# Performance work log

Measured on AMD Instinct MI355X. Metric: run time of the kernel, lower is better.

Reference implementation:

```python
import jax, jax.numpy as jnp
import numpy as np

P = 16          # patch size
GH = GW = 29    # grid (464/16)
N = GH * GW     # 841 tokens
E = 384         # embed dim
NH = 6          # heads
HD = E // NH    # 64
DEPTH = 8
EPS = 1e-5


def _dist_bias():
    g = jnp.linspace(0.0, 1.0, GH)
    gy, gx = jnp.meshgrid(g, g, indexing='ij')
    coords = jnp.stack([gy.ravel(), gx.ravel()], axis=-1)        # [N,2]
    d2 = ((coords[None, :, :] - coords[:, None, :]) ** 2).sum(-1)  # [N,N]
    return -d2 / d2.max()                                        # in [-1,0]


def _ln(x, g, b):
    m = x.mean(-1, keepdims=True)
    v = ((x - m) ** 2).mean(-1, keepdims=True)
    return (x - m) * jax.lax.rsqrt(v + EPS) * g + b


def _shift(x, dy, dx):
    # zero-pad shift, matching F.pad default 'constant' mode in the source
    B, C, H, W = x.shape
    if dy > 0:
        x = jnp.pad(x, ((0, 0), (0, 0), (dy, 0), (0, 0)))[:, :, :H, :]
    elif dy < 0:
        x = jnp.pad(x, ((0, 0), (0, 0), (0, -dy), (0, 0)))[:, :, -H:, :]
    if dx > 0:
        x = jnp.pad(x, ((0, 0), (0, 0), (0, 0), (dx, 0)))[:, :, :, :W]
    elif dx < 0:
        x = jnp.pad(x, ((0, 0), (0, 0), (0, 0), (0, -dx)))[:, :, :, -W:]
    return x


def _patchify(x):
    B, C, H, W = x.shape
    gh, gw = H // P, W // P
    x = x.reshape(B, C, gh, P, gw, P)
    x = x.transpose(0, 2, 4, 1, 3, 5)         # [B,gh,gw,C,p,p]
    return x.reshape(B, gh * gw, C * P * P)


def setup_inputs() -> dict:
    key = jax.random.key(0)
    ks = jax.random.split(key, 8)
    D = DEPTH
    s = 0.02
    inp = {
        'x': jax.random.normal(ks[0], (16, 3, 464, 464), jnp.float32),
        'tok_ng': jnp.ones((3840,), jnp.float32),
        'tok_nb': jnp.zeros((3840,), jnp.float32),
        'tok_w1': jax.random.normal(ks[1], (3840, 768), jnp.float32) * s,
        'tok_b1': jnp.zeros((768,), jnp.float32),
        'tok_w2': jax.random.normal(ks[2], (768, 384), jnp.float32) * s,
        'tok_b2': jnp.zeros((384,), jnp.float32),
        'ln1_g': jnp.ones((D, E), jnp.float32),
        'ln1_b': jnp.zeros((D, E), jnp.float32),
        'w_qkv': jax.random.normal(ks[3], (D, E, 3 * E), jnp.float32) * s,
        'temp': jnp.full((D, NH), np.log(HD ** -0.5), jnp.float32),
        'loc_w': jnp.full((D, NH), 0.1, jnp.float32),
        'w_proj': jax.random.normal(ks[4], (D, E, E), jnp.float32) * s,
        'b_proj': jnp.zeros((D, E), jnp.float32),
        'ls1': jnp.full((D, E), 1e-4, jnp.float32),
        'ln2_g': jnp.ones((D, E), jnp.float32),
        'ln2_b': jnp.zeros((D, E), jnp.float32),
        'ff_w1': jax.random.normal(ks[5], (D, E, 4 * E), jnp.float32) * s,
        'ff_b1': jnp.zeros((D, 4 * E), jnp.float32),
        'ff_w2': jax.random.normal(ks[6], (D, 4 * E, E), jnp.float32) * s,
        'ff_b2': jnp.zeros((D, E), jnp.float32),
        'ls2': jnp.full((D, E), 1e-4, jnp.float32),
    }
    return inp


def _forward(x, tok_ng, tok_nb, tok_w1, tok_b1, tok_w2, tok_b2,
             ln1_g, ln1_b, w_qkv, temp, loc_w, w_proj, b_proj, ls1,
             ln2_g, ln2_b, ff_w1, ff_b1, ff_w2, ff_b2, ls2):
    p2 = P // 2
    shifts = [x, _shift(x, p2, 0), _shift(x, -p2, 0), _shift(x, 0, p2), _shift(x, 0, -p2)]
    patches = jnp.concatenate([_patchify(s) for s in shifts], axis=-1)  # [B,N,3840]
    h = _ln(patches, tok_ng, tok_nb)
    h = jax.nn.gelu(h @ tok_w1 + tok_b1, approximate=False)
    h = h @ tok_w2 + tok_b2                                             # [B,N,E]

    loc = _dist_bias()                                                  # [N,N]

    def block(h, p):
        (g1, b1, wqkv, tp, lw, wp, bp, l1, g2, b2, fw1, fb1, fw2, fb2, l2) = p
        y = _ln(h, g1, b1)
        qkv = (y @ wqkv).reshape(h.shape[0], N, 3, NH, HD)
        qkv = qkv.transpose(2, 0, 3, 1, 4)                              # [3,B,H,N,hd]
        q, k, v = qkv[0], qkv[1], qkv[2]
        scale = jnp.exp(tp)[:, None, None]                              # per-head temperature
        logits = jnp.einsum('bhnd,bhmd->bhnm', q, k) * scale
        logits = logits + lw[:, None, None] * loc                       # per-head locality bias
        a = jax.nn.softmax(logits, axis=-1)
        o = jnp.einsum('bhnm,bhmd->bhnd', a, v)
        o = o.transpose(0, 2, 1, 3).reshape(h.shape[0], N, E)
        h = h + l1 * (o @ wp + bp)
        y2 = _ln(h, g2, b2)
        f = jax.nn.gelu(y2 @ fw1 + fb1, approximate=False) @ fw2 + fb2
        h = h + l2 * f
        return h, None

    params = (ln1_g, ln1_b, w_qkv, temp, loc_w, w_proj, b_proj, ls1,
              ln2_g, ln2_b, ff_w1, ff_b1, ff_w2, ff_b2, ls2)
    h, _ = jax.lax.scan(block, h, params)
    return h


def reference(x, tok_ng, tok_nb, tok_w1, tok_b1, tok_w2, tok_b2,
              ln1_g, ln1_b, w_qkv, temp, loc_w, w_proj, b_proj, ls1,
              ln2_g, ln2_b, ff_w1, ff_b1, ff_w2, ff_b2, ls2):
    return _forward(x, tok_ng, tok_nb, tok_w1, tok_b1, tok_w2, tok_b2,
                    ln1_g, ln1_b, w_qkv, temp, loc_w, w_proj, b_proj, ls1,
                    ln2_g, ln2_b, ff_w1, ff_b1, ff_w2, ff_b2, ls2)
```

## Files before the change

### kernel.cpp

```cpp
#include <hip/hip_runtime.h>
#include <math.h>

typedef __attribute__((ext_vector_type(8))) short short8;
typedef __attribute__((ext_vector_type(4))) float f32x4;
typedef unsigned short u16;

#define NTOK 841
#define GRID_H 29
#define E_ 384
#define NH_ 6
#define MROWS 13456
#define MP 13568
#define MQ 14336
#define CM 5120

__device__ __forceinline__ u16 f2bf(float f) {
  union { float f; unsigned int u; } c; c.f = f;
  unsigned int u = c.u;
  return (u16)((u + 0x7fffu + ((u >> 16) & 1u)) >> 16);
}

__device__ __forceinline__ float bf2f(u16 b) {
  union { unsigned int u; float f; } c; c.u = ((unsigned int)b) << 16; return c.f;
}

__device__ __forceinline__ float gelu_exact(float v) {
  return 0.5f * v * (1.f + erff(v * 0.70710678118654752440f));
}

__device__ __forceinline__ float fexp2(float x) {
  float r; asm("v_exp_f32 %0, %1" : "=v"(r) : "v"(x)); return r;
}

__device__ __forceinline__ int swz64(int row, int col) {
  return row * 128 + ((((col >> 3) ^ (row & 7)) << 4) | ((col & 7) << 1));
}

__global__ __launch_bounds__(256) void transpose_conv(const float* __restrict__ in,
    u16* __restrict__ out, int K, int N) {
  __shared__ float tile[32][33];
  size_t zo = (size_t)blockIdx.z * K * N;
  const float* inp = in + zo;
  u16* outp = out + zo;
  int n0 = blockIdx.x * 32, k0 = blockIdx.y * 32;
  int tx = threadIdx.x & 31, ty = threadIdx.x >> 5;
  #pragma unroll
  for (int r = ty; r < 32; r += 8) tile[r][tx] = inp[(size_t)(k0 + r) * N + n0 + tx];
  __syncthreads();
  #pragma unroll
  for (int r = ty; r < 32; r += 8) outp[(size_t)(n0 + r) * K + k0 + tx] = f2bf(tile[tx][r]);
}

__global__ __launch_bounds__(256) void patch_ln(const float* __restrict__ x,
    const float* __restrict__ g, const float* __restrict__ bsh, u16* __restrict__ out,
    int t0) {
  int t = t0 + blockIdx.x;
  int tid = threadIdx.x;
  u16* orow = out + (size_t)blockIdx.x * 3840;
  if (t >= MROWS) {
    #pragma unroll
    for (int j = 0; j < 15; ++j) orow[tid + j * 256] = 0;
    return;
  }
  int bimg = t / NTOK, n = t % NTOK;
  int gy = n / GRID_H, gx = n % GRID_H;
  float vals[15];
  float s1 = 0.f, s2 = 0.f;
  #pragma unroll
  for (int j = 0; j < 15; ++j) {
    int cout = tid + j * 256;
    int s = cout / 768, rem = cout % 768;
    int c = rem / 256, rem2 = rem % 256;
    int py = rem2 / 16, px = rem2 % 16;
    int dy = (s == 1 ? 8 : 0) - (s == 2 ? 8 : 0);
    int dx = (s == 3 ? 8 : 0) - (s == 4 ? 8 : 0);
    int Y = gy * 16 + py - dy;
    int X = gx * 16 + px - dx;
    float v = 0.f;
    if (Y >= 0 && Y < 464 && X >= 0 && X < 464)
      v = x[(((size_t)bimg * 3 + c) * 464 + Y) * 464 + X];
    vals[j] = v;
    s1 += v; s2 += v * v;
  }
  #pragma unroll
  for (int m = 1; m < 64; m <<= 1) { s1 += __shfl_xor(s1, m); s2 += __shfl_xor(s2, m); }
  __shared__ float ws1[4], ws2[4];
  int wid = tid >> 6;
  if ((tid & 63) == 0) { ws1[wid] = s1; ws2[wid] = s2; }
  __syncthreads();
  s1 = ws1[0] + ws1[1] + ws1[2] + ws1[3];
  s2 = ws2[0] + ws2[1] + ws2[2] + ws2[3];
  float mean = s1 * (1.f / 3840.f);
  float var = s2 * (1.f / 3840.f) - mean * mean;
  float rs = rsqrtf(var + 1e-5f);
  #pragma unroll
  for (int j = 0; j < 15; ++j) {
    int cout = tid + j * 256;
    orow[cout] = f2bf((vals[j] - mean) * rs * g[cout] + bsh[cout]);
  }
}

__global__ __launch_bounds__(256) void ln384(const float* __restrict__ h,
    const float* __restrict__ g, const float* __restrict__ bsh, u16* __restrict__ y) {
  int row = blockIdx.x * 4 + (threadIdx.x >> 6);
  int lane = threadIdx.x & 63;
  const float* hr = h + (size_t)row * E_;
  float v[6];
  float s1 = 0.f;
  #pragma unroll
  for (int j = 0; j < 6; ++j) { v[j] = hr[lane + j * 64]; s1 += v[j]; }
  #pragma unroll
  for (int m = 1; m < 64; m <<= 1) s1 += __shfl_xor(s1, m);
  float mean = s1 * (1.f / 384.f);
  float s2 = 0.f;
  #pragma unroll
  for (int j = 0; j < 6; ++j) { float d = v[j] - mean; s2 += d * d; }
  #pragma unroll
  for (int m = 1; m < 64; m <<= 1) s2 += __shfl_xor(s2, m);
  float rs = rsqrtf(s2 * (1.f / 384.f) + 1e-5f);
  u16* yr = y + (size_t)row * E_;
  #pragma unroll
  for (int j = 0; j < 6; ++j) {
    int c = lane + j * 64;
    yr[c] = f2bf((v[j] - mean) * rs * g[c] + bsh[c]);
  }
}

__global__ __launch_bounds__(256) void ln384p(const float* __restrict__ h,
    const float* __restrict__ g, const float* __restrict__ bsh, u16* __restrict__ yp) {
  int rowp = blockIdx.x * 4 + (threadIdx.x >> 6);
  int lane = threadIdx.x & 63;
  int bg = rowp / 896, tk = rowp - bg * 896;
  u16* yr = yp + (size_t)rowp * E_;
  if (tk >= NTOK) {
    #pragma unroll
    for (int j = 0; j < 6; ++j) yr[lane + j * 64] = 0;
    return;
  }
  const float* hr = h + (size_t)(bg * NTOK + tk) * E_;
  float v[6];
  float s1 = 0.f;
  #pragma unroll
  for (int j = 0; j < 6; ++j) { v[j] = hr[lane + j * 64]; s1 += v[j]; }
  #pragma unroll
  for (int m = 1; m < 64; m <<= 1) s1 += __shfl_xor(s1, m);
  float mean = s1 * (1.f / 384.f);
  float s2 = 0.f;
  #pragma unroll
  for (int j = 0; j < 6; ++j) { float d = v[j] - mean; s2 += d * d; }
  #pragma unroll
  for (int m = 1; m < 64; m <<= 1) s2 += __shfl_xor(s2, m);
  float rs = rsqrtf(s2 * (1.f / 384.f) + 1e-5f);
  #pragma unroll
  for (int j = 0; j < 6; ++j) {
    int c = lane + j * 64;
    yr[c] = f2bf((v[j] - mean) * rs * g[c] + bsh[c]);
  }
}

template<int EPI, int TM>
__global__ __launch_bounds__(256) void gemm_bt(
    const u16* __restrict__ A, const u16* __restrict__ BT,
    int N, int K,
    const float* __restrict__ bias, const float* __restrict__ lscale,
    float* __restrict__ resid, u16* __restrict__ outb, float* __restrict__ outf) {
  constexpr int MI = TM / 32;
  constexpr int BUF = (TM + 128) * 64;
  __shared__ alignas(16) char smem[2 * BUF * 2];
  short* As = (short*)smem;
  const int gx = gridDim.x;
  const int nwg = gx * gridDim.y;
  int L = blockIdx.x + blockIdx.y * gx;
  int q8 = nwg >> 3, r8 = nwg & 7, xcd = L & 7, pos = L >> 3;
  int L2 = (xcd < r8 ? xcd * (q8 + 1) : r8 * (q8 + 1) + (xcd - r8) * q8) + pos;
  const int m0 = (L2 / gx) * TM, n0 = (L2 % gx) * 128;
  const int tid = threadIdx.x;
  const int lane = tid & 63, wid = tid >> 6;
  const int wm = wid >> 1, wn = wid & 1;
  const int rowl = lane >> 3;
  const int colc = (((lane & 7) ^ (rowl & 7)) << 3);
  f32x4 acc[MI][4] = {};
  const int nkt = K >> 6;

  auto stage = [&](int b, int kt) {
    short* Ab = As + b * BUF;
    short* Bb = Ab + TM * 64;
    const int k0 = kt * 64;
    #pragma unroll
    for (int i = 0; i < TM / 32; ++i) {
      int chunk = i * 4 + wid;
      const u16* ga = A + (size_t)(m0 + chunk * 8 + rowl) * K + k0 + colc;
      __builtin_amdgcn_global_load_lds((const __attribute__((address_space(1))) void*)ga,
          (__attribute__((address_space(3))) void*)(Ab + (chunk << 9)), 16, 0, 0);
    }
    #pragma unroll
    for (int i = 0; i < 4; ++i) {
      int chunk = i * 4 + wid;
      const u16* gb = BT + (size_t)(n0 + chunk * 8 + rowl) * K + k0 + colc;
      __builtin_amdgcn_global_load_lds((const __attribute__((address_space(1))) void*)gb,
          (__attribute__((address_space(3))) void*)(Bb + (chunk << 9)), 16, 0, 0);
    }
  };

  stage(0, 0);
  for (int kt = 0; kt < nkt; ++kt) {
    const int cur = kt & 1;
    if (kt + 1 < nkt) {
      stage(cur ^ 1, kt + 1);
      if (TM == 128) asm volatile("s_waitcnt vmcnt(8)" ::: "memory");
      else           asm volatile("s_waitcnt vmcnt(6)" ::: "memory");
    } else {
      asm volatile("s_waitcnt vmcnt(0)" ::: "memory");
    }
    __builtin_amdgcn_s_barrier();
    __builtin_amdgcn_sched_barrier(0);
    short* Ab = As + cur * BUF;
    short* Bb = Ab + TM * 64;
    #pragma unroll
    for (int kk = 0; kk < 2; ++kk) {
      short8 a[MI], bfr[4];
      #pragma unroll
      for (int mi = 0; mi < MI; ++mi) {
        int ra = wm * (TM / 2) + mi * 16 + (lane & 15);
        a[mi] = *(const short8*)(Ab + ra * 64 + ((((kk << 2) | (lane >> 4)) ^ (ra & 7)) << 3));
      }
      #pragma unroll
      for (int nj = 0; nj < 4; ++nj) {
        int rb = wn * 64 + nj * 16 + (lane & 15);
        bfr[nj] = *(const short8*)(Bb + rb * 64 + ((((kk << 2) | (lane >> 4)) ^ (rb & 7)) << 3));
      }
      #pragma unroll
      for (int mi = 0; mi < MI; ++mi)
        #pragma unroll
        for (int nj = 0; nj < 4; ++nj)
          acc[mi][nj] = __builtin_amdgcn_mfma_f32_16x16x32_bf16(a[mi], bfr[nj], acc[mi][nj], 0, 0, 0);
    }
    __builtin_amdgcn_s_barrier();
  }
  const int rrow = (lane >> 4) << 2;
  const int ccol = lane & 15;
  if (EPI == 1) {
    u16* Cs = (u16*)smem;
    __syncthreads();
    #pragma unroll
    for (int mi = 0; mi < MI; ++mi)
      #pragma unroll
      for (int nj = 0; nj < 4; ++nj) {
        int cc = wn * 64 + nj * 16 + ccol;
        float bi = bias[n0 + cc];
        #pragma unroll
        for (int r = 0; r < 4; ++r) {
          int cr = wm * (TM / 2) + mi * 16 + rrow + r;
          Cs[cr * 136 + cc] = f2bf(gelu_exact(acc[mi][nj][r] + bi));
        }
      }
    __syncthreads();
    #pragma unroll
    for (int it = 0; it < TM / 16; ++it) {
      int idx = it * 256 + tid;
      int orow = idx >> 4, c = idx & 15;
      short8 v = *(const short8*)(Cs + orow * 136 + c * 8);
      *(short8*)(outb + (size_t)(m0 + orow) * N + n0 + c * 8) = v;
    }
    return;
  }
  #pragma unroll
  for (int mi = 0; mi < MI; ++mi)
    #pragma unroll
    for (int nj = 0; nj < 4; ++nj) {
      int gn = n0 + wn * 64 + nj * 16 + ccol;
      #pragma unroll
      for (int r = 0; r < 4; ++r) {
        int gm = m0 + wm * (TM / 2) + mi * 16 + rrow + r;
        float v = acc[mi][nj][r];
        if (EPI == 2) {
          outf[(size_t)gm * N + gn] = v + bias[gn];
        } else {
          float* p = resid + (size_t)gm * N + gn;
          *p = *p + lscale[gn] * (v + bias[gn]);
        }
      }
    }
}

__global__ __launch_bounds__(256) void gemm_qkv(
    const u16* __restrict__ A, const u16* __restrict__ BT,
    u16* __restrict__ Qp, u16* __restrict__ Kp, u16* __restrict__ Vp) {
  const int K = 384;
  constexpr int BUF = 256 * 64;
  __shared__ alignas(16) char smem[2 * BUF * 2];
  short* As = (short*)smem;
  int L = blockIdx.x + blockIdx.y * 9;
  int L2 = (L & 7) * 126 + (L >> 3);
  const int m0 = (L2 / 9) * 128, n0 = (L2 % 9) * 128;
  const int tid = threadIdx.x;
  const int lane = tid & 63, wid = tid >> 6;
  const int wm = wid >> 1, wn = wid & 1;
  const int rowl = lane >> 3;
  const int colc = (((lane & 7) ^ (rowl & 7)) << 3);
  f32x4 acc[4][4] = {};

  auto stage = [&](int b, int kt) {
    short* Ab = As + b * BUF;
    short* Bb = Ab + 128 * 64;
    const int k0 = kt * 64;
    #pragma unroll
    for (int i = 0; i < 4; ++i) {
      int chunk = i * 4 + wid;
      const u16* ga = A + (size_t)(m0 + chunk * 8 + rowl) * K + k0 + colc;
      __builtin_amdgcn_global_load_lds((const __attribute__((address_space(1))) void*)ga,
          (__attribute__((address_space(3))) void*)(Ab + (chunk << 9)), 16, 0, 0);
      const u16* gb = BT + (size_t)(n0 + chunk * 8 + rowl) * K + k0 + colc;
      __builtin_amdgcn_global_load_lds((const __attribute__((address_space(1))) void*)gb,
          (__attribute__((address_space(3))) void*)(Bb + (chunk << 9)), 16, 0, 0);
    }
  };

  stage(0, 0);
  for (int kt = 0; kt < 6; ++kt) {
    const int cur = kt & 1;
    if (kt + 1 < 6) {
      stage(cur ^ 1, kt + 1);
      asm volatile("s_waitcnt vmcnt(8)" ::: "memory");
    } else {
      asm volatile("s_waitcnt vmcnt(0)" ::: "memory");
    }
    __builtin_amdgcn_s_barrier();
    __builtin_amdgcn_sched_barrier(0);
    short* Ab = As + cur * BUF;
    short* Bb = Ab + 128 * 64;
    #pragma unroll
    for (int kk = 0; kk < 2; ++kk) {
      short8 a[4], bfr[4];
      #pragma unroll
      for (int mi = 0; mi < 4; ++mi) {
        int ra = wm * 64 + mi * 16 + (lane & 15);
        a[mi] = *(const short8*)(Ab + ra * 64 + ((((kk << 2) | (lane >> 4)) ^ (ra & 7)) << 3));
      }
      #pragma unroll
      for (int nj = 0; nj < 4; ++nj) {
        int rb = wn * 64 + nj * 16 + (lane & 15);
        bfr[nj] = *(const short8*)(Bb + rb * 64 + ((((kk << 2) | (lane >> 4)) ^ (rb & 7)) << 3));
      }
      #pragma unroll
      for (int mi = 0; mi < 4; ++mi)
        #pragma unroll
        for (int nj = 0; nj < 4; ++nj)
          acc[mi][nj] = __builtin_amdgcn_mfma_f32_16x16x32_bf16(a[mi], bfr[nj], acc[mi][nj], 0, 0, 0);
    }
    __builtin_amdgcn_s_barrier();
  }
  const int seg = n0 / 384;
  const int h0 = (n0 - seg * 384) >> 6;
  const int bg = m0 / 896;
  const int tk0 = m0 - bg * 896;
  const int rrow = (lane >> 4) << 2;
  const int ccol = lane & 15;
  u16* Cs = (u16*)smem;
  __syncthreads();
  #pragma unroll
  for (int mi = 0; mi < 4; ++mi)
    #pragma unroll
    for (int nj = 0; nj < 4; ++nj) {
      int cc = wn * 64 + nj * 16 + ccol;
      #pragma unroll
      for (int r = 0; r < 4; ++r) {
        int cr = wm * 64 + mi * 16 + rrow + r;
        u16 bv = f2bf(acc[mi][nj][r]);
        if (seg == 2) Cs[cc * 136 + cr] = bv;
        else          Cs[cr * 136 + cc] = bv;
      }
    }
  __syncthreads();
  #pragma unroll
  for (int i = 0; i < 8; ++i) {
    int idx = i * 256 + tid;
    int c = idx & 7;
    int orow = idx >> 3;
    int hs = orow >> 7;
    int rl = orow & 127;
    size_t bh = (size_t)(bg * 6 + h0 + hs);
    if (seg == 2) {
      int tile_l = rl >> 6, hd = rl & 63;
      short8 v = *(const short8*)(Cs + (hs * 64 + hd) * 136 + tile_l * 64 + c * 8);
      int tile = (tk0 >> 6) + tile_l;
      *(short8*)(Vp + bh * 57344 + tile * 4096 + hd * 64 + ((c ^ (hd & 7)) << 3)) = v;
    } else {
      short8 v = *(const short8*)(Cs + rl * 136 + hs * 64 + c * 8);
      if (seg == 0) {
        *(short8*)(Qp + (bh * 896 + tk0 + rl) * 64 + c * 8) = v;
      } else {
        int tok = tk0 + rl;
        *(short8*)(Kp + bh * 57344 + (tok >> 6) * 4096 + (tok & 63) * 64 + ((c ^ (tok & 7)) << 3)) = v;
      }
    }
  }
}

__global__ __launch_bounds__(256) void attn_sk(const u16* __restrict__ Qp,
    const u16* __restrict__ Kp, const u16* __restrict__ Vp,
    const float* __restrict__ temp_d, const float* __restrict__ locw_d,
    u16* __restrict__ op, float* __restrict__ ml) {
  int Lw = blockIdx.x;
  int L2 = (Lw & 7) * 336 + (Lw >> 3);
  const int bh = L2 / 28;
  const int rem = L2 % 28;
  const int ks = rem / 14, qt = rem % 14;
  const int hh = bh % NH_;
  const int tid = threadIdx.x, lane = tid & 63, w = tid >> 6;
  const int lg = lane >> 4, lc = lane & 15;
  const float LOG2E = 1.44269504088896f;
  const float scale = __expf(temp_d[hh]) * LOG2E;
  const float lwh = locw_d[hh] * LOG2E * -0.5f;
  const int kb0 = ks * 448;

  __shared__ alignas(16) char ktl[2][8192];
  __shared__ alignas(16) char vtl[2][8192];
  __shared__ alignas(16) char pl[4][2048];
  __shared__ float yx2[896 * 2];

  for (int j = tid; j < 896; j += 256) {
    unsigned jc = j < NTOK ? (unsigned)j : (NTOK - 1);
    yx2[j * 2]     = (float)(jc / 29u) * (1.f / 28.f);
    yx2[j * 2 + 1] = (float)(jc % 29u) * (1.f / 28.f);
  }

  const char* qb = (const char*)(Qp + ((size_t)bh * 896 + qt * 64) * 64);
  short8 qf0 = *(const short8*)(qb + (w * 16 + lc) * 128 + lg * 16);
  short8 qf1 = *(const short8*)(qb + (w * 16 + lc) * 128 + 64 + lg * 16);

  const char* kbase = (const char*)Kp + ((size_t)bh * 14 + ks * 7) * 8192;
  const char* vbase = (const char*)Vp + ((size_t)bh * 14 + ks * 7) * 8192;

  auto stage = [&](int b, int kt) {
    #pragma unroll
    for (int i = 0; i < 2; ++i) {
      int off = (i * 4 + w) * 1024;
      __builtin_amdgcn_global_load_lds(
          (const __attribute__((address_space(1))) void*)(kbase + kt * 8192 + off + lane * 16),
          (__attribute__((address_space(3))) void*)(ktl[b] + off), 16, 0, 0);
      __builtin_amdgcn_global_load_lds(
          (const __attribute__((address_space(1))) void*)(vbase + kt * 8192 + off + lane * 16),
          (__attribute__((address_space(3))) void*)(vtl[b] + off), 16, 0, 0);
    }
  };

  f32x4 of[4] = {};
  float mrow[4], psum[4];
  #pragma unroll
  for (int r = 0; r < 4; ++r) { mrow[r] = -3e38f; psum[r] = 0.f; }

  stage(0, 0);
  asm volatile("s_waitcnt vmcnt(0)" ::: "memory");
  __syncthreads();

  float qy[4], qx[4];
  #pragma unroll
  for (int r = 0; r < 4; ++r) {
    int iq = qt * 64 + w * 16 + (lg << 2) + r;
    qy[r] = yx2[iq * 2];
    qx[r] = yx2[iq * 2 + 1];
  }

  for (int kt = 0; kt < 7; ++kt) {
    const int b = kt & 1;
    if (kt < 6) stage(b ^ 1, kt + 1);

    const char* kb = ktl[b];
    const char* vb = vtl[b];
    f32x4 sf[4];
    __builtin_amdgcn_s_setprio(1);
    #pragma unroll
    for (int nt = 0; nt < 4; ++nt) {
      short8 kf0 = *(const short8*)(kb + swz64(nt * 16 + lc, lg << 3));
      short8 kf1 = *(const short8*)(kb + swz64(nt * 16 + lc, 32 + (lg << 3)));
      f32x4 z = {0.f, 0.f, 0.f, 0.f};
      z = __builtin_amdgcn_mfma_f32_16x16x32_bf16(qf0, kf0, z, 0, 0, 0);
      z = __builtin_amdgcn_mfma_f32_16x16x32_bf16(qf1, kf1, z, 0, 0, 0);
      sf[nt] = z;
    }
    __builtin_amdgcn_s_setprio(0);

    const int jb = kb0 + kt * 64;
    #pragma unroll
    for (int nt = 0; nt < 4; ++nt) {
      int j = jb + nt * 16 + lc;
      float jy = yx2[j * 2], jx = yx2[j * 2 + 1];
      #pragma unroll
      for (int r = 0; r < 4; ++r) {
        float dy = qy[r] - jy, dx = qx[r] - jx;
        sf[nt][r] = sf[nt][r] * scale + lwh * (dy * dy + dx * dx);
      }
    }
    if (jb + 64 > NTOK) {
      #pragma unroll
      for (int nt = 0; nt < 4; ++nt) {
        if (jb + nt * 16 + lc >= NTOK) {
          sf[nt][0] = -3e38f; sf[nt][1] = -3e38f; sf[nt][2] = -3e38f; sf[nt][3] = -3e38f;
        }
      }
    }

    float lm[4];
    #pragma unroll
    for (int r = 0; r < 4; ++r)
      lm[r] = fmaxf(fmaxf(sf[0][r], sf[1][r]), fmaxf(sf[2][r], sf[3][r]));
    bool trig = (lm[0] > mrow[0] + 12.f) | (lm[1] > mrow[1] + 12.f) |
                (lm[2] > mrow[2] + 12.f) | (lm[3] > mrow[3] + 12.f);
    if (__any(trig)) {
      #pragma unroll
      for (int r = 0; r < 4; ++r) {
        float tm = lm[r];
        #pragma unroll
        for (int m = 1; m < 16; m <<= 1) tm = fmaxf(tm, __shfl_xor(tm, m));
        float mnew = fmaxf(mrow[r], tm);
        float alpha = fexp2(mrow[r] - mnew);
        psum[r] *= alpha;
        of[0][r] *= alpha; of[1][r] *= alpha; of[2][r] *= alpha; of[3][r] *= alpha;
        mrow[r] = mnew;
      }
    }

    char* plw = pl[w];
    #pragma unroll
    for (int nt = 0; nt < 4; ++nt)
      #pragma unroll
      for (int r = 0; r < 4; ++r) {
        float p = fexp2(sf[nt][r] - mrow[r]);
        psum[r] += p;
        *(u16*)(plw + swz64((lg << 2) + r, nt * 16 + lc)) = f2bf(p);
      }
    asm volatile("s_waitcnt lgkmcnt(0)" ::: "memory");
    __builtin_amdgcn_sched_barrier(0);
    short8 pa[2];
    #pragma unroll
    for (int t = 0; t < 2; ++t)
      pa[t] = *(const short8*)(plw + swz64(lc, t * 32 + (lg << 3)));

    __builtin_amdgcn_s_setprio(1);
    #pragma unroll
    for (int n2 = 0; n2 < 4; ++n2) {
      f32x4 accv = of[n2];
      #pragma unroll
      for (int t = 0; t < 2; ++t) {
        short8 vf = *(const short8*)(vb + swz64(n2 * 16 + lc, t * 32 + (lg << 3)));
        accv = __builtin_amdgcn_mfma_f32_16x16x32_bf16(pa[t], vf, accv, 0, 0, 0);
      }
      of[n2] = accv;
    }
    __builtin_amdgcn_s_setprio(0);

    if (kt < 6) {
      asm volatile("s_waitcnt vmcnt(0) lgkmcnt(0)" ::: "memory");
      __builtin_amdgcn_sched_barrier(0);
      __builtin_amdgcn_s_barrier();
    }
  }

  #pragma unroll
  for (int r = 0; r < 4; ++r) {
    float s = psum[r];
    #pragma unroll
    for (int m = 1; m < 16; m <<= 1) s += __shfl_xor(s, m);
    int iq = qt * 64 + w * 16 + (lg << 2) + r;
    if (iq < NTOK) {
      size_t rb = (size_t)(ks * 96 + bh) * 896 + iq;
      #pragma unroll
      for (int n2 = 0; n2 < 4; ++n2)
        op[rb * 64 + n2 * 16 + lc] = f2bf(of[n2][r]);
      if (lc == 0) { ml[rb * 2] = mrow[r]; ml[rb * 2 + 1] = s; }
    }
  }
}

__global__ __launch_bounds__(256) void combine(const u16* __restrict__ op,
    const float* __restrict__ ml, u16* __restrict__ ob) {
  const int bh = blockIdx.y, bimg = bh / NH_, hh = bh % NH_;
  const int wid = threadIdx.x >> 6, lane = threadIdx.x & 63;
  const int tokb = blockIdx.x * 16 + wid * 4;
  #pragma unroll
  for (int rr = 0; rr < 4; ++rr) {
    int tok = tokb + rr;
    if (tok >= NTOK) return;
    size_t i1 = (size_t)bh * 896 + tok;
    size_t i2 = (size_t)(96 + bh) * 896 + tok;
    float m1 = ml[i1 * 2], l1 = ml[i1 * 2 + 1];
    float m2 = ml[i2 * 2], l2 = ml[i2 * 2 + 1];
    float m = fmaxf(m1, m2);
    float w1 = fexp2(m1 - m), w2 = fexp2(m2 - m);
    float inv = 1.f / (l1 * w1 + l2 * w2);
    float o1 = bf2f(op[i1 * 64 + lane]);
    float o2 = bf2f(op[i2 * 64 + lane]);
    ob[((size_t)(bimg * NTOK + tok)) * E_ + hh * 64 + lane] =
        f2bf((o1 * w1 + o2 * w2) * inv);
  }
}

__global__ __launch_bounds__(256) void copy_out(const float* __restrict__ h, float* __restrict__ out) {
  size_t i = (size_t)blockIdx.x * 256 + threadIdx.x;
  if (i < (size_t)MROWS * E_) out[i] = h[i];
}

extern "C" void kernel_launch(void* const* d_in, const int* in_sizes, int n_in,
                              void* d_out, int out_size, void* d_ws, size_t ws_size,
                              hipStream_t stream) {
  const float* x      = (const float*)d_in[0];
  const float* tok_ng = (const float*)d_in[1];
  const float* tok_nb = (const float*)d_in[2];
  const float* tok_w1 = (const float*)d_in[3];
  const float* tok_b1 = (const float*)d_in[4];
  const float* tok_w2 = (const float*)d_in[5];
  const float* tok_b2 = (const float*)d_in[6];
  const float* ln1_g  = (const float*)d_in[7];
  const float* ln1_b  = (const float*)d_in[8];
  const float* w_qkv  = (const float*)d_in[9];
  const float* temp   = (const float*)d_in[10];
  const float* loc_w  = (const float*)d_in[11];
  const float* w_proj = (const float*)d_in[12];
  const float* b_proj = (const float*)d_in[13];
  const float* ls1    = (const float*)d_in[14];
  const float* ln2_g  = (const float*)d_in[15];
  const float* ln2_b  = (const float*)d_in[16];
  const float* ff_w1  = (const float*)d_in[17];
  const float* ff_b1  = (const float*)d_in[18];
  const float* ff_w2  = (const float*)d_in[19];
  const float* ff_b2  = (const float*)d_in[20];
  const float* ls2    = (const float*)d_in[21];
  float* out = (float*)d_out;

  char* ws = (char*)d_ws;
  size_t off = 0;
  auto alloc = [&](size_t bytes) -> void* {
    void* p = ws + off; off += (bytes + 255) & ~(size_t)255; return p;
  };
  u16* w1T   = (u16*)alloc(768UL * 3840 * 2);
  u16* w2T   = (u16*)alloc(384UL * 768 * 2);
  u16* qkvT  = (u16*)alloc(8UL * 1152 * 384 * 2);
  u16* projT = (u16*)alloc(8UL * 384 * 384 * 2);
  u16* f1T   = (u16*)alloc(8UL * 1536 * 384 * 2);
  u16* f2T   = (u16*)alloc(8UL * 384 * 1536 * 2);
  float* h   = (float*)alloc((size_t)MP * 384 * 4);
  char* regB = (char*)alloc(22500000);
  u16* h1   = (u16*)regB;
  u16* ypad = (u16*)regB;
  u16* yff  = (u16*)regB;
  u16* ob   = (u16*)(regB + 11010048);
  char* regA = (char*)alloc((size_t)MP * 1536 * 2);
  u16* Xlnc = (u16*)regA;
  u16* Qp   = (u16*)regA;
  u16* Kp   = (u16*)(regA + 11010048);
  u16* Vp   = (u16*)(regA + 22020096);
  u16* f1b  = (u16*)regA;
  u16* op   = (u16*)alloc(2UL * 96 * 896 * 64 * 2);
  float* ml = (float*)alloc(2UL * 96 * 896 * 2 * 4);
  (void)in_sizes; (void)n_in; (void)out_size;

  if (off > ws_size) return;

  transpose_conv<<<dim3(24, 120, 1), 256, 0, stream>>>(tok_w1, w1T, 3840, 768);
  transpose_conv<<<dim3(12, 24, 1), 256, 0, stream>>>(tok_w2, w2T, 768, 384);
  transpose_conv<<<dim3(36, 12, 8), 256, 0, stream>>>(w_qkv, qkvT, 384, 1152);
  transpose_conv<<<dim3(12, 12, 8), 256, 0, stream>>>(w_proj, projT, 384, 384);
  transpose_conv<<<dim3(48, 12, 8), 256, 0, stream>>>(ff_w1, f1T, 384, 1536);
  transpose_conv<<<dim3(12, 48, 8), 256, 0, stream>>>(ff_w2, f2T, 1536, 384);

  for (int m = 0; m < MP; m += CM) {
    int rows = MP - m; if (rows > CM) rows = CM;
    patch_ln<<<rows, 256, 0, stream>>>(x, tok_ng, tok_nb, Xlnc, m);
    gemm_bt<1, 128><<<dim3(6, rows / 128), 256, 0, stream>>>(Xlnc, w1T, 768, 3840,
        tok_b1, nullptr, nullptr, h1 + (size_t)m * 768, nullptr);
  }
  gemm_bt<2, 64><<<dim3(3, MP / 64), 256, 0, stream>>>(h1, w2T, 384, 768, tok_b2,
      nullptr, nullptr, nullptr, h);

  for (int d = 0; d < 8; ++d) {
    ln384p<<<MQ / 4, 256, 0, stream>>>(h, ln1_g + d * E_, ln1_b + d * E_, ypad);
    gemm_qkv<<<dim3(9, 112), 256, 0, stream>>>(ypad, qkvT + (size_t)d * 1152 * 384, Qp, Kp, Vp);
    attn_sk<<<2688, 256, 0, stream>>>(Qp, Kp, Vp, temp + d * NH_, loc_w + d * NH_, op, ml);
    combine<<<dim3(53, 96), 256, 0, stream>>>(op, ml, ob);
    gemm_bt<3, 64><<<dim3(3, MP / 64), 256, 0, stream>>>(ob, projT + (size_t)d * 384 * 384,
        384, 384, b_proj + d * E_, ls1 + d * E_, h, nullptr, nullptr);
    ln384<<<MP / 4, 256, 0, stream>>>(h, ln2_g + d * E_, ln2_b + d * E_, yff);
    gemm_bt<1, 128><<<dim3(12, MP / 128), 256, 0, stream>>>(yff, f1T + (size_t)d * 1536 * 384,
        1536, 384, ff_b1 + d * 1536, nullptr, nullptr, f1b, nullptr);
    gemm_bt<3, 64><<<dim3(3, MP / 64), 256, 0, stream>>>(f1b, f2T + (size_t)d * 384 * 1536,
        384, 1536, ff_b2 + d * E_, ls2 + d * E_, h, nullptr, nullptr);
  }

  copy_out<<<(MROWS * E_ + 255) / 256, 256, 0, stream>>>(h, out);
}
```

Measured before the change: 1.897 ms.

## Drop split-K attention and combine kernel; process full key range per block

Attention no longer splits the key range into two halves. Each block now loops over all 14 key tiles and normalizes its output directly into the projection input. This removes the separate combine kernel and the bf16 partial-output and max/sum round trip through global memory. In exchange the grid shrinks from 2688 to 1344 blocks, so each block runs a longer serial loop and there is less parallelism to hide latency.

```diff
diff --git a/kernel.cpp b/kernel.cpp
--- a/kernel.cpp
+++ b/kernel.cpp
@@ -397,22 +397,19 @@
   }
 }
 
-__global__ __launch_bounds__(256) void attn_sk(const u16* __restrict__ Qp,
+__global__ __launch_bounds__(256) void attn_sp(const u16* __restrict__ Qp,
     const u16* __restrict__ Kp, const u16* __restrict__ Vp,
     const float* __restrict__ temp_d, const float* __restrict__ locw_d,
-    u16* __restrict__ op, float* __restrict__ ml) {
+    u16* __restrict__ ob) {
   int Lw = blockIdx.x;
-  int L2 = (Lw & 7) * 336 + (Lw >> 3);
-  const int bh = L2 / 28;
-  const int rem = L2 % 28;
-  const int ks = rem / 14, qt = rem % 14;
+  int L2 = (Lw & 7) * 168 + (Lw >> 3);
+  const int bh = L2 / 14, qt = L2 % 14;
   const int hh = bh % NH_;
   const int tid = threadIdx.x, lane = tid & 63, w = tid >> 6;
   const int lg = lane >> 4, lc = lane & 15;
   const float LOG2E = 1.44269504088896f;
   const float scale = __expf(temp_d[hh]) * LOG2E;
   const float lwh = locw_d[hh] * LOG2E * -0.5f;
-  const int kb0 = ks * 448;
 
   __shared__ alignas(16) char ktl[2][8192];
   __shared__ alignas(16) char vtl[2][8192];
@@ -429,8 +426,8 @@
   short8 qf0 = *(const short8*)(qb + (w * 16 + lc) * 128 + lg * 16);
   short8 qf1 = *(const short8*)(qb + (w * 16 + lc) * 128 + 64 + lg * 16);
 
-  const char* kbase = (const char*)Kp + ((size_t)bh * 14 + ks * 7) * 8192;
-  const char* vbase = (const char*)Vp + ((size_t)bh * 14 + ks * 7) * 8192;
+  const char* kbase = (const char*)Kp + (size_t)bh * 14 * 8192;
+  const char* vbase = (const char*)Vp + (size_t)bh * 14 * 8192;
 
   auto stage = [&](int b, int kt) {
     #pragma unroll
@@ -462,9 +459,9 @@
     qx[r] = yx2[iq * 2 + 1];
   }
 
-  for (int kt = 0; kt < 7; ++kt) {
+  for (int kt = 0; kt < 14; ++kt) {
     const int b = kt & 1;
-    if (kt < 6) stage(b ^ 1, kt + 1);
+    if (kt < 13) stage(b ^ 1, kt + 1);
 
     const char* kb = ktl[b];
     const char* vb = vtl[b];
@@ -481,7 +478,7 @@
     }
     __builtin_amdgcn_s_setprio(0);
 
-    const int jb = kb0 + kt * 64;
+    const int jb = kt * 64;
     #pragma unroll
     for (int nt = 0; nt < 4; ++nt) {
       int j = jb + nt * 16 + lc;
@@ -550,13 +547,14 @@
     }
     __builtin_amdgcn_s_setprio(0);
 
-    if (kt < 6) {
+    if (kt < 13) {
       asm volatile("s_waitcnt vmcnt(0) lgkmcnt(0)" ::: "memory");
       __builtin_amdgcn_sched_barrier(0);
       __builtin_amdgcn_s_barrier();
     }
   }
 
+  const int bimg = bh / NH_;
   #pragma unroll
   for (int r = 0; r < 4; ++r) {
     float s = psum[r];
@@ -564,35 +562,12 @@
     for (int m = 1; m < 16; m <<= 1) s += __shfl_xor(s, m);
     int iq = qt * 64 + w * 16 + (lg << 2) + r;
     if (iq < NTOK) {
-      size_t rb = (size_t)(ks * 96 + bh) * 896 + iq;
+      float rl = 1.f / s;
       #pragma unroll
       for (int n2 = 0; n2 < 4; ++n2)
-        op[rb * 64 + n2 * 16 + lc] = f2bf(of[n2][r]);
-      if (lc == 0) { ml[rb * 2] = mrow[r]; ml[rb * 2 + 1] = s; }
-    }
-  }
-}
-
-__global__ __launch_bounds__(256) void combine(const u16* __restrict__ op,
-    const float* __restrict__ ml, u16* __restrict__ ob) {
-  const int bh = blockIdx.y, bimg = bh / NH_, hh = bh % NH_;
-  const int wid = threadIdx.x >> 6, lane = threadIdx.x & 63;
-  const int tokb = blockIdx.x * 16 + wid * 4;
-  #pragma unroll
-  for (int rr = 0; rr < 4; ++rr) {
-    int tok = tokb + rr;
-    if (tok >= NTOK) return;
-    size_t i1 = (size_t)bh * 896 + tok;
-    size_t i2 = (size_t)(96 + bh) * 896 + tok;
-    float m1 = ml[i1 * 2], l1 = ml[i1 * 2 + 1];
-    float m2 = ml[i2 * 2], l2 = ml[i2 * 2 + 1];
-    float m = fmaxf(m1, m2);
-    float w1 = fexp2(m1 - m), w2 = fexp2(m2 - m);
-    float inv = 1.f / (l1 * w1 + l2 * w2);
-    float o1 = bf2f(op[i1 * 64 + lane]);
-    float o2 = bf2f(op[i2 * 64 + lane]);
-    ob[((size_t)(bimg * NTOK + tok)) * E_ + hh * 64 + lane] =
-        f2bf((o1 * w1 + o2 * w2) * inv);
+        ob[((size_t)(bimg * NTOK + iq)) * E_ + hh * 64 + n2 * 16 + lc] =
+            f2bf(of[n2][r] * rl);
+    }
   }
 }
 
@@ -651,8 +626,6 @@
   u16* Kp   = (u16*)(regA + 11010048);
   u16* Vp   = (u16*)(regA + 22020096);
   u16* f1b  = (u16*)regA;
-  u16* op   = (u16*)alloc(2UL * 96 * 896 * 64 * 2);
-  float* ml = (float*)alloc(2UL * 96 * 896 * 2 * 4);
   (void)in_sizes; (void)n_in; (void)out_size;
 
   if (off > ws_size) return;
@@ -676,8 +649,7 @@
   for (int d = 0; d < 8; ++d) {
     ln384p<<<MQ / 4, 256, 0, stream>>>(h, ln1_g + d * E_, ln1_b + d * E_, ypad);
     gemm_qkv<<<dim3(9, 112), 256, 0, stream>>>(ypad, qkvT + (size_t)d * 1152 * 384, Qp, Kp, Vp);
-    attn_sk<<<2688, 256, 0, stream>>>(Qp, Kp, Vp, temp + d * NH_, loc_w + d * NH_, op, ml);
-    combine<<<dim3(53, 96), 256, 0, stream>>>(op, ml, ob);
+    attn_sp<<<1344, 256, 0, stream>>>(Qp, Kp, Vp, temp + d * NH_, loc_w + d * NH_, ob);
     gemm_bt<3, 64><<<dim3(3, MP / 64), 256, 0, stream>>>(ob, projT + (size_t)d * 384 * 384,
         384, 384, b_proj + d * E_, ls1 + d * E_, h, nullptr, nullptr);
     ln384<<<MP / 4, 256, 0, stream>>>(h, ln2_g + d * E_, ln2_b + d * E_, yff);
```

New measurement: 1.775 ms. 1.07x faster.
